# Kernel tuning notes

Hardware: AMD Instinct MI355X
Metric: run time of the kernel (lower is better)

The kernel has to match this reference:

```python
import jax, jax.numpy as jnp
import numpy as np

B, S, D, H, V, C = 64, 512, 512, 512, 32000, 1000
FF = 1024

def setup_inputs() -> dict:
    key = jax.random.key(0)
    ks = jax.random.split(key, 12)
    s = 0.02
    return {
        "tokens": jax.random.randint(ks[0], (B, S), 0, V),
        "emb": jax.random.normal(ks[1], (V, D), jnp.float32) * s,
        "Wx": jax.random.normal(ks[2], (D, H), jnp.float32) * s,
        "Wh": jax.random.normal(ks[3], (H, H), jnp.float32) * s,
        "b_rnn": jnp.zeros((H,), jnp.float32),
        "W1": jax.random.normal(ks[4], (H, FF), jnp.float32) * s,
        "b1": jnp.zeros((FF,), jnp.float32),
        "W2": jax.random.normal(ks[5], (FF, FF), jnp.float32) * s,
        "b2": jnp.zeros((FF,), jnp.float32),
        "Wo": jax.random.normal(ks[6], (FF, C), jnp.float32) * s,
        "bo": jnp.zeros((C,), jnp.float32),
    }

def reference(tokens, emb, Wx, Wh, b_rnn, W1, b1, W2, b2, Wo, bo):
    # Embedding with mask_zero=True: token 0 is a masked timestep
    x = emb[tokens]                                   # [B,S,D]
    mask = (tokens != 0)                              # [B,S]
    # Precompute input projection for all timesteps (hoisted out of the scan)
    xproj = jnp.einsum('bsd,dh->bsh', x, Wx) + b_rnn  # [B,S,H]

    def step(h, inp):
        xp, m = inp                                   # [B,H], [B]
        h_new = jax.nn.relu(xp + h @ Wh)
        # Keras masking: masked steps carry previous state forward
        h = jnp.where(m[:, None], h_new, h)
        return h, None

    h0 = jnp.zeros((B, H), xproj.dtype)
    h, _ = jax.lax.scan(step, h0, (xproj.transpose(1, 0, 2), mask.T))

    y = jax.nn.relu(h @ W1 + b1)
    y = jax.nn.relu(y @ W2 + b2)
    return jax.nn.softmax(y @ Wo + bo, axis=-1)       # [B,C]
```

## Files before the change

### kernel.cpp

```cpp
#include <hip/hip_runtime.h>
#include <stdint.h>

typedef _Float16 half2_t __attribute__((ext_vector_type(2)));
typedef short bf16x8 __attribute__((ext_vector_type(8)));
typedef float f32x4 __attribute__((ext_vector_type(4)));
typedef int i32x4 __attribute__((ext_vector_type(4)));
typedef int i32x8 __attribute__((ext_vector_type(8)));
typedef unsigned short u16;
typedef unsigned int u32;
typedef unsigned long long u64;

#define B_ 64
#define S_ 512
#define D_ 512
#define H_ 512
#define FF_ 1024
#define C_ 1000
#define V_ 32000

#define SW4 128.0f
#define SH4 256.0f

__device__ __forceinline__ u16 f2bf(float f){
  u32 u = __builtin_bit_cast(u32, f);
  u = (u + 0x7FFFu + ((u >> 16) & 1u)) >> 16;
  return (u16)u;
}
__device__ __forceinline__ u32 pkbf(float a, float b){
  return (u32)f2bf(a) | ((u32)f2bf(b) << 16);
}
__device__ __forceinline__ u32 packh2(float a, float b){
  u16 lo = __builtin_bit_cast(u16, (_Float16)a);
  u16 hi = __builtin_bit_cast(u16, (_Float16)b);
  return (u32)lo | ((u32)hi << 16);
}
__device__ __forceinline__ float fdot2u(u32 a, u32 b, float c){
  return __builtin_amdgcn_fdot2(__builtin_bit_cast(half2_t, a),
                                __builtin_bit_cast(half2_t, b), c, false);
}
__device__ __forceinline__ float h2f(u16 h){
  return (float)__builtin_bit_cast(_Float16, h);
}
__device__ __forceinline__ float fp4val(u32 c){
  int e = (c >> 1) & 3;
  float m = 1.0f + 0.5f * (float)(c & 1);
  return (e == 0) ? 0.5f * (float)(c & 1) : m * (float)(1 << (e - 1));
}

__global__ void k_prep(const float* __restrict__ Wx, u16* __restrict__ WxT,
                       const float* __restrict__ Wh, uint4* __restrict__ Wf4,
                       const float* __restrict__ W1, u32* __restrict__ W1p,
                       const float* __restrict__ W2, u32* __restrict__ W2p,
                       const float* __restrict__ Wo, u32* __restrict__ Wop){
  __shared__ u16 t[64][65];
  int bid = blockIdx.x, tid = threadIdx.x;
  if (bid < 64){
    int bx = bid & 7, by = bid >> 3;
    int c = tid & 63, r0 = (tid >> 6) * 16;
    #pragma unroll
    for (int i = 0; i < 16; i++){
      int k = by * 64 + r0 + i, n = bx * 64 + c;
      t[r0 + i][c] = f2bf(Wx[k * 512 + n]);
    }
    __syncthreads();
    #pragma unroll
    for (int i = 0; i < 16; i++){
      int n = bx * 64 + r0 + i, k = by * 64 + c;
      WxT[n * 512 + k] = t[c][r0 + i];
    }
  } else if (bid < 96){
    int g = (bid - 64) * 256 + tid;
    int fidx = g >> 6, l = g & 63;
    int wv = fidx >> 4, ct = (fidx >> 2) & 3, kt = fidx & 3;
    int q = l >> 4, n = wv * 64 + ct * 16 + (l & 15);
    int k0 = kt * 128 + q * 32;
    u32 d[4] = {0u, 0u, 0u, 0u};
    #pragma unroll
    for (int j = 0; j < 32; j++){
      float w = Wh[(size_t)(k0 + j) * 512 + n] * SW4;
      float aw = fabsf(w);
      u32 s = (w < 0.f) ? 8u : 0u;
      u32 c;
      if (aw < 2.f) c = (u32)(int)rintf(aw * 2.f);
      else if (aw < 4.f) c = 4u + (u32)(int)rintf(aw - 2.f);
      else { c = 6u + (u32)(int)rintf((aw - 4.f) * 0.5f); if (c > 7u) c = 7u; }
      d[j >> 3] |= (c | s) << (4 * (j & 7));
    }
    uint4 o; o.x = d[0]; o.y = d[1]; o.z = d[2]; o.w = d[3];
    Wf4[(size_t)fidx * 64 + l] = o;
  } else if (bid < 1120){
    int b2 = bid - 96;
    int p = b2 >> 2, n = (b2 & 3) * 256 + tid;
    W1p[p * FF_ + n] = packh2(W1[(2 * p) * FF_ + n], W1[(2 * p + 1) * FF_ + n]);
  } else if (bid < 3168){
    int b2 = bid - 1120;
    int p = b2 >> 2, n = (b2 & 3) * 256 + tid;
    W2p[p * FF_ + n] = packh2(W2[(2 * p) * FF_ + n], W2[(2 * p + 1) * FF_ + n]);
  } else {
    int b2 = bid - 3168;
    int p = b2 >> 2, n = (b2 & 3) * 256 + tid;
    if (n < C_)
      Wop[p * C_ + n] = packh2(Wo[(2 * p) * C_ + n], Wo[(2 * p + 1) * C_ + n]);
  }
}

__global__ __launch_bounds__(512) void k_gemm(const float* __restrict__ emb,
                                              const u16* __restrict__ WxT,
                                              const float* __restrict__ bias,
                                              u16* __restrict__ xpV){
  __shared__ __align__(16) u16 As[64 * 40];
  int tid = threadIdx.x;
  int m0 = blockIdx.x * 64;
  int w = tid >> 6, l = tid & 63, kg = l >> 4, r16 = l & 15;
  const u16* bptr[4];
  #pragma unroll
  for (int ni = 0; ni < 4; ni++)
    bptr[ni] = WxT + (size_t)(w * 64 + ni * 16 + r16) * 512 + kg * 8;
  f32x4 acc[4][4];
  #pragma unroll
  for (int mi = 0; mi < 4; mi++)
    #pragma unroll
    for (int ni = 0; ni < 4; ni++) acc[mi][ni] = (f32x4){0.f, 0.f, 0.f, 0.f};
  int srow = tid >> 3, sk = (tid & 7) * 4;
  for (int kt = 0; kt < 16; kt++){
    float4 f = *(const float4*)(emb + (size_t)(m0 + srow) * 512 + kt * 32 + sk);
    u32 lo = pkbf(f.x, f.y), hi = pkbf(f.z, f.w);
    __syncthreads();
    uint2 st; st.x = lo; st.y = hi;
    *(uint2*)(As + srow * 40 + sk) = st;
    __syncthreads();
    bf16x8 bfr[4], af[4];
    #pragma unroll
    for (int ni = 0; ni < 4; ni++)
      bfr[ni] = *(const bf16x8*)(bptr[ni] + kt * 32);
    #pragma unroll
    for (int mi = 0; mi < 4; mi++)
      af[mi] = *(const bf16x8*)(As + (mi * 16 + r16) * 40 + kg * 8);
    #pragma unroll
    for (int mi = 0; mi < 4; mi++)
      #pragma unroll
      for (int ni = 0; ni < 4; ni++)
        acc[mi][ni] = __builtin_amdgcn_mfma_f32_16x16x32_bf16(af[mi], bfr[ni], acc[mi][ni], 0, 0, 0);
  }
  #pragma unroll
  for (int ni = 0; ni < 4; ni++){
    int col = w * 64 + ni * 16 + r16;
    float bb = bias[col];
    #pragma unroll
    for (int mi = 0; mi < 4; mi++){
      int mb = m0 + mi * 16 + kg * 4;
      #pragma unroll
      for (int r = 0; r < 4; r++){
        float v = (acc[mi][ni][r] + bb) * SH4;
        xpV[(size_t)(mb + r) * 512 + col] = __builtin_bit_cast(u16, (_Float16)v);
      }
    }
  }
}

__global__ __launch_bounds__(512, 2) void k_rnn(
    const uint4* __restrict__ Wf4, const u16* __restrict__ xpV,
    const int* __restrict__ tokens, u32* __restrict__ hpack){
  __shared__ __align__(16) unsigned char g4[2][256];
  __shared__ int toks[512];
  int b = blockIdx.x, tid = threadIdx.x;
  int wv = tid >> 6, l = tid & 63, q = l >> 4, n16 = l & 15;
  int col = wv * 64 + q * 16 + n16;

  i32x8 wgt[16];
  #pragma unroll
  for (int ct = 0; ct < 4; ct++)
    #pragma unroll
    for (int kt = 0; kt < 4; kt++){
      int fidx = (wv * 4 + ct) * 4 + kt;
      uint4 wl = Wf4[(size_t)fidx * 64 + l];
      i32x8 w8 = {(int)wl.x, (int)wl.y, (int)wl.z, (int)wl.w, 0, 0, 0, 0};
      wgt[ct * 4 + kt] = w8;
    }

  toks[tid] = tokens[b * 512 + tid];
  if (tid < 64) ((u32*)g4[0])[tid] = 0;
  __syncthreads();

  u16 xraw = xpV[(size_t)toks[0] * 512 + col];
  u32 greg = 0;

  #pragma unroll 1
  for (int t = 0; t < 512; t++){
    int tn = toks[t < 511 ? t + 1 : 0];
    u16 xnext = xpV[(size_t)tn * 512 + col];
    bool wr = toks[t] != 0;
    const unsigned char* gc = g4[t & 1];

    f32x4 acc0 = {0.f,0.f,0.f,0.f}, acc1 = {0.f,0.f,0.f,0.f};
    f32x4 acc2 = {0.f,0.f,0.f,0.f}, acc3 = {0.f,0.f,0.f,0.f};
    #pragma unroll
    for (int kt = 0; kt < 4; kt++){
      i32x4 av = *(const i32x4*)(gc + kt * 64 + q * 16);
      i32x8 a8 = {av[0], av[1], av[2], av[3], 0, 0, 0, 0};
      acc0 = __builtin_amdgcn_mfma_scale_f32_16x16x128_f8f6f4(
          a8, wgt[0 * 4 + kt], acc0, 4, 4, 0, 127, 0, 127);
      acc1 = __builtin_amdgcn_mfma_scale_f32_16x16x128_f8f6f4(
          a8, wgt[1 * 4 + kt], acc1, 4, 4, 0, 127, 0, 127);
      acc2 = __builtin_amdgcn_mfma_scale_f32_16x16x128_f8f6f4(
          a8, wgt[2 * 4 + kt], acc2, 4, 4, 0, 127, 0, 127);
      acc3 = __builtin_amdgcn_mfma_scale_f32_16x16x128_f8f6f4(
          a8, wgt[3 * 4 + kt], acc3, 4, 4, 0, 127, 0, 127);
    }

    float av = (q == 0) ? acc0[0] : (q == 1) ? acc1[0] : (q == 2) ? acc2[0] : acc3[0];
    float gn = fmaxf(fmaf(av, 1.0f / SW4, h2f(xraw)), 0.f);
    u32 code;
    if (gn < 2.f) code = (u32)(int)rintf(gn * 2.f);
    else if (gn < 4.f) code = 4u + (u32)(int)rintf(gn - 2.f);
    else { u32 c = 6u + (u32)(int)rintf((gn - 4.f) * 0.5f); code = c > 7u ? 7u : c; }
    u32 pc = (u32)__shfl_xor((int)code, 1);
    u32 byte = (n16 & 1) ? (pc | (code << 4)) : (code | (pc << 4));
    if (wr) greg = byte;
    if ((l & 1) == 0) g4[(t + 1) & 1][col >> 1] = (unsigned char)greg;
    xraw = xnext;
    __syncthreads();
  }

  if (tid < 256){
    u32 byte = g4[0][tid];
    float f0 = fp4val(byte & 15u) * (1.0f / SH4);
    float f1 = fp4val(byte >> 4) * (1.0f / SH4);
    hpack[b * 256 + tid] = packh2(f0, f1);
  }
}

__global__ __launch_bounds__(512) void k_tail(const u32* __restrict__ hpack,
    const u32* __restrict__ W1p, const float* __restrict__ b1v,
    const u32* __restrict__ W2p, const float* __restrict__ b2v,
    const u32* __restrict__ Wop, const float* __restrict__ bov,
    float* __restrict__ out){
  __shared__ __align__(16) u32 A0[256], A1[256];
  __shared__ __align__(16) u32 B0[512], B1[512];
  __shared__ __align__(16) u32 C0[512], C1[512];
  __shared__ float redm0[8], redm1[8], reds0[8], reds1[8];
  int ba = blockIdx.x * 2, bb = ba + 1;
  int tid = threadIdx.x, wv = tid >> 6;
  if (tid < 256){ A0[tid] = hpack[ba * 256 + tid]; A1[tid] = hpack[bb * 256 + tid]; }
  __syncthreads();

  float a00 = 0.f, a01 = 0.f, a10 = 0.f, a11 = 0.f;
  #pragma unroll 4
  for (int p = 0; p < 256; p += 2){
    u32 h00 = A0[p], h01 = A0[p + 1], h10 = A1[p], h11 = A1[p + 1];
    const u32* wp = W1p + (size_t)p * FF_ + tid;
    u32 w0 = wp[0], w1 = wp[512], w0b = wp[FF_], w1b = wp[FF_ + 512];
    a00 = fdot2u(w0, h00, a00);  a01 = fdot2u(w1, h00, a01);
    a10 = fdot2u(w0, h10, a10);  a11 = fdot2u(w1, h10, a11);
    a00 = fdot2u(w0b, h01, a00); a01 = fdot2u(w1b, h01, a01);
    a10 = fdot2u(w0b, h11, a10); a11 = fdot2u(w1b, h11, a11);
  }
  {
    float blo = b1v[tid], bhi = b1v[tid + 512];
    float y00 = fmaxf(a00 + blo, 0.f), y01 = fmaxf(a01 + bhi, 0.f);
    float y10 = fmaxf(a10 + blo, 0.f), y11 = fmaxf(a11 + bhi, 0.f);
    float o00 = __shfl_xor(y00, 1), o01 = __shfl_xor(y01, 1);
    float o10 = __shfl_xor(y10, 1), o11 = __shfl_xor(y11, 1);
    if (!(tid & 1)){
      int i = tid >> 1;
      B0[i] = packh2(y00, o00); B0[256 + i] = packh2(y01, o01);
      B1[i] = packh2(y10, o10); B1[256 + i] = packh2(y11, o11);
    }
  }
  __syncthreads();

  a00 = a01 = a10 = a11 = 0.f;
  #pragma unroll 4
  for (int p = 0; p < 512; p += 2){
    u32 h00 = B0[p], h01 = B0[p + 1], h10 = B1[p], h11 = B1[p + 1];
    const u32* wp = W2p + (size_t)p * FF_ + tid;
    u32 w0 = wp[0], w1 = wp[512], w0b = wp[FF_], w1b = wp[FF_ + 512];
    a00 = fdot2u(w0, h00, a00);  a01 = fdot2u(w1, h00, a01);
    a10 = fdot2u(w0, h10, a10);  a11 = fdot2u(w1, h10, a11);
    a00 = fdot2u(w0b, h01, a00); a01 = fdot2u(w1b, h01, a01);
    a10 = fdot2u(w0b, h11, a10); a11 = fdot2u(w1b, h11, a11);
  }
  {
    float blo = b2v[tid], bhi = b2v[tid + 512];
    float y00 = fmaxf(a00 + blo, 0.f), y01 = fmaxf(a01 + bhi, 0.f);
    float y10 = fmaxf(a10 + blo, 0.f), y11 = fmaxf(a11 + bhi, 0.f);
    float o00 = __shfl_xor(y00, 1), o01 = __shfl_xor(y01, 1);
    float o10 = __shfl_xor(y10, 1), o11 = __shfl_xor(y11, 1);
    if (!(tid & 1)){
      int i = tid >> 1;
      C0[i] = packh2(y00, o00); C0[256 + i] = packh2(y01, o01);
      C1[i] = packh2(y10, o10); C1[256 + i] = packh2(y11, o11);
    }
  }
  __syncthreads();

  int n1 = tid + 512;
  bool v1 = n1 < C_;
  int n1c = v1 ? n1 : 0;
  float z00 = 0.f, z01 = 0.f, z10 = 0.f, z11 = 0.f;
  #pragma unroll 4
  for (int p = 0; p < 512; p++){
    u32 y0 = C0[p], y1 = C1[p];
    u32 w0 = Wop[(size_t)p * C_ + tid], w1 = Wop[(size_t)p * C_ + n1c];
    z00 = fdot2u(w0, y0, z00); z01 = fdot2u(w1, y0, z01);
    z10 = fdot2u(w0, y1, z10); z11 = fdot2u(w1, y1, z11);
  }
  z00 += bov[tid]; z10 += bov[tid];
  z01 += bov[n1c]; z11 += bov[n1c];
  float mx0 = fmaxf(z00, v1 ? z01 : -1e30f);
  float mx1 = fmaxf(z10, v1 ? z11 : -1e30f);
  #pragma unroll
  for (int o = 1; o < 64; o <<= 1){
    mx0 = fmaxf(mx0, __shfl_xor(mx0, o));
    mx1 = fmaxf(mx1, __shfl_xor(mx1, o));
  }
  if ((tid & 63) == 0){ redm0[wv] = mx0; redm1[wv] = mx1; }
  __syncthreads();
  mx0 = redm0[0]; mx1 = redm1[0];
  #pragma unroll
  for (int i = 1; i < 8; i++){
    mx0 = fmaxf(mx0, redm0[i]);
    mx1 = fmaxf(mx1, redm1[i]);
  }
  float e00 = __expf(z00 - mx0), e01 = v1 ? __expf(z01 - mx0) : 0.f;
  float e10 = __expf(z10 - mx1), e11 = v1 ? __expf(z11 - mx1) : 0.f;
  float s0 = e00 + e01, s1 = e10 + e11;
  #pragma unroll
  for (int o = 1; o < 64; o <<= 1){
    s0 += __shfl_xor(s0, o);
    s1 += __shfl_xor(s1, o);
  }
  if ((tid & 63) == 0){ reds0[wv] = s0; reds1[wv] = s1; }
  __syncthreads();
  s0 = 0.f; s1 = 0.f;
  #pragma unroll
  for (int i = 0; i < 8; i++){ s0 += reds0[i]; s1 += reds1[i]; }
  float inv0 = 1.0f / s0, inv1 = 1.0f / s1;
  out[(size_t)ba * C_ + tid] = e00 * inv0;
  out[(size_t)bb * C_ + tid] = e10 * inv1;
  if (v1){
    out[(size_t)ba * C_ + n1] = e01 * inv0;
    out[(size_t)bb * C_ + n1] = e11 * inv1;
  }
}

extern "C" void kernel_launch(void* const* d_in, const int* in_sizes, int n_in,
                              void* d_out, int out_size, void* d_ws, size_t ws_size,
                              hipStream_t stream) {
  const int*   tokens = (const int*)d_in[0];
  const float* emb    = (const float*)d_in[1];
  const float* Wx     = (const float*)d_in[2];
  const float* Wh     = (const float*)d_in[3];
  const float* brnn   = (const float*)d_in[4];
  const float* W1     = (const float*)d_in[5];
  const float* b1     = (const float*)d_in[6];
  const float* W2     = (const float*)d_in[7];
  const float* b2     = (const float*)d_in[8];
  const float* Wo     = (const float*)d_in[9];
  const float* bo     = (const float*)d_in[10];
  float* out = (float*)d_out;

  char* ws = (char*)d_ws;
  size_t off = 0;
  auto alloc = [&](size_t bytes) -> void* {
    void* p = ws + off;
    off += (bytes + 255) & ~(size_t)255;
    return p;
  };
  u16* WxT    = (u16*)alloc((size_t)512 * 512 * 2);
  u16* xpV    = (u16*)alloc((size_t)V_ * 512 * 2);
  uint4* Wf4  = (uint4*)alloc((size_t)128 * 64 * 16);
  u32* W1p    = (u32*)alloc((size_t)256 * 1024 * 4);
  u32* W2p    = (u32*)alloc((size_t)512 * 1024 * 4);
  u32* Wop    = (u32*)alloc((size_t)512 * 1000 * 4);
  u32* hpack  = (u32*)alloc((size_t)64 * 256 * 4);

  k_prep<<<dim3(5216), dim3(256), 0, stream>>>(Wx, WxT, Wh, Wf4,
                                               W1, W1p, W2, W2p, Wo, Wop);
  k_gemm<<<dim3(500), dim3(512), 0, stream>>>(emb, WxT, brnn, xpV);
  k_rnn<<<dim3(64), dim3(512), 0, stream>>>(Wf4, xpV, tokens, hpack);
  k_tail<<<dim3(32), dim3(512), 0, stream>>>(hpack, W1p, b1, W2p, b2, Wop, bo, out);
}
```

Baseline: 413.2 us.

## Split tail MLP into multi-block kernels and fold weight packing into GEMM launch

The single 32-block tail kernel, which ran FC1, FC2, the output projection and the softmax serially per batch pair, is replaced by four kernels. Each layer now spreads its output columns over a 4x32 grid, followed by a separate softmax kernel, so more CUs share the weight streaming. Packing of W1/W2/Wo moves from k_prep into extra blocks of the embedding GEMM launch, so it runs alongside the GEMM, and the GEMM software-prefetches the next emb tile. The cost is extra launches and intermediate round-trips through global memory.

```diff
diff --git a/kernel.cpp b/kernel.cpp
--- a/kernel.cpp
+++ b/kernel.cpp
@@ -48,10 +48,7 @@
 }
 
 __global__ void k_prep(const float* __restrict__ Wx, u16* __restrict__ WxT,
-                       const float* __restrict__ Wh, uint4* __restrict__ Wf4,
-                       const float* __restrict__ W1, u32* __restrict__ W1p,
-                       const float* __restrict__ W2, u32* __restrict__ W2p,
-                       const float* __restrict__ Wo, u32* __restrict__ Wop){
+                       const float* __restrict__ Wh, uint4* __restrict__ Wf4){
   __shared__ u16 t[64][65];
   int bid = blockIdx.x, tid = threadIdx.x;
   if (bid < 64){
@@ -68,7 +65,7 @@
       int n = bx * 64 + r0 + i, k = by * 64 + c;
       WxT[n * 512 + k] = t[c][r0 + i];
     }
-  } else if (bid < 96){
+  } else {
     int g = (bid - 64) * 256 + tid;
     int fidx = g >> 6, l = g & 63;
     int wv = fidx >> 4, ct = (fidx >> 2) & 3, kt = fidx & 3;
@@ -88,29 +85,36 @@
     }
     uint4 o; o.x = d[0]; o.y = d[1]; o.z = d[2]; o.w = d[3];
     Wf4[(size_t)fidx * 64 + l] = o;
-  } else if (bid < 1120){
-    int b2 = bid - 96;
-    int p = b2 >> 2, n = (b2 & 3) * 256 + tid;
-    W1p[p * FF_ + n] = packh2(W1[(2 * p) * FF_ + n], W1[(2 * p + 1) * FF_ + n]);
-  } else if (bid < 3168){
-    int b2 = bid - 1120;
-    int p = b2 >> 2, n = (b2 & 3) * 256 + tid;
-    W2p[p * FF_ + n] = packh2(W2[(2 * p) * FF_ + n], W2[(2 * p + 1) * FF_ + n]);
-  } else {
-    int b2 = bid - 3168;
-    int p = b2 >> 2, n = (b2 & 3) * 256 + tid;
-    if (n < C_)
-      Wop[p * C_ + n] = packh2(Wo[(2 * p) * C_ + n], Wo[(2 * p + 1) * C_ + n]);
   }
 }
 
 __global__ __launch_bounds__(512) void k_gemm(const float* __restrict__ emb,
                                               const u16* __restrict__ WxT,
                                               const float* __restrict__ bias,
-                                              u16* __restrict__ xpV){
+                                              u16* __restrict__ xpV,
+                                              const float* __restrict__ W1, u32* __restrict__ W1p,
+                                              const float* __restrict__ W2, u32* __restrict__ W2p,
+                                              const float* __restrict__ Wo, u32* __restrict__ Wop){
   __shared__ __align__(16) u16 As[64 * 40];
-  int tid = threadIdx.x;
-  int m0 = blockIdx.x * 64;
+  int bid = blockIdx.x, tid = threadIdx.x;
+  if (bid >= 500){
+    if (bid < 1012){
+      int i = (bid - 500) * 512 + tid;
+      int p = i >> 10, n = i & 1023;
+      W1p[p * FF_ + n] = packh2(W1[(2 * p) * FF_ + n], W1[(2 * p + 1) * FF_ + n]);
+    } else if (bid < 2036){
+      int i = (bid - 1012) * 512 + tid;
+      int p = i >> 10, n = i & 1023;
+      W2p[p * FF_ + n] = packh2(W2[(2 * p) * FF_ + n], W2[(2 * p + 1) * FF_ + n]);
+    } else {
+      int i = (bid - 2036) * 512 + tid;
+      int p = i >> 10, n = i & 1023;
+      if (n < C_)
+        Wop[p * C_ + n] = packh2(Wo[(2 * p) * C_ + n], Wo[(2 * p + 1) * C_ + n]);
+    }
+    return;
+  }
+  int m0 = bid * 64;
   int w = tid >> 6, l = tid & 63, kg = l >> 4, r16 = l & 15;
   const u16* bptr[4];
   #pragma unroll
@@ -122,9 +126,12 @@
     #pragma unroll
     for (int ni = 0; ni < 4; ni++) acc[mi][ni] = (f32x4){0.f, 0.f, 0.f, 0.f};
   int srow = tid >> 3, sk = (tid & 7) * 4;
+  const float* ebase = emb + (size_t)(m0 + srow) * 512 + sk;
+  float4 f = *(const float4*)ebase;
   for (int kt = 0; kt < 16; kt++){
-    float4 f = *(const float4*)(emb + (size_t)(m0 + srow) * 512 + kt * 32 + sk);
     u32 lo = pkbf(f.x, f.y), hi = pkbf(f.z, f.w);
+    float4 fn;
+    if (kt < 15) fn = *(const float4*)(ebase + (kt + 1) * 32);
     __syncthreads();
     uint2 st; st.x = lo; st.y = hi;
     *(uint2*)(As + srow * 40 + sk) = st;
@@ -141,6 +148,7 @@
       #pragma unroll
       for (int ni = 0; ni < 4; ni++)
         acc[mi][ni] = __builtin_amdgcn_mfma_f32_16x16x32_bf16(af[mi], bfr[ni], acc[mi][ni], 0, 0, 0);
+    f = fn;
   }
   #pragma unroll
   for (int ni = 0; ni < 4; ni++){
@@ -230,118 +238,108 @@
   }
 }
 
-__global__ __launch_bounds__(512) void k_tail(const u32* __restrict__ hpack,
-    const u32* __restrict__ W1p, const float* __restrict__ b1v,
-    const u32* __restrict__ W2p, const float* __restrict__ b2v,
-    const u32* __restrict__ Wop, const float* __restrict__ bov,
-    float* __restrict__ out){
-  __shared__ __align__(16) u32 A0[256], A1[256];
-  __shared__ __align__(16) u32 B0[512], B1[512];
-  __shared__ __align__(16) u32 C0[512], C1[512];
-  __shared__ float redm0[8], redm1[8], reds0[8], reds1[8];
-  int ba = blockIdx.x * 2, bb = ba + 1;
-  int tid = threadIdx.x, wv = tid >> 6;
-  if (tid < 256){ A0[tid] = hpack[ba * 256 + tid]; A1[tid] = hpack[bb * 256 + tid]; }
-  __syncthreads();
-
-  float a00 = 0.f, a01 = 0.f, a10 = 0.f, a11 = 0.f;
-  #pragma unroll 4
-  for (int p = 0; p < 256; p += 2){
-    u32 h00 = A0[p], h01 = A0[p + 1], h10 = A1[p], h11 = A1[p + 1];
-    const u32* wp = W1p + (size_t)p * FF_ + tid;
-    u32 w0 = wp[0], w1 = wp[512], w0b = wp[FF_], w1b = wp[FF_ + 512];
-    a00 = fdot2u(w0, h00, a00);  a01 = fdot2u(w1, h00, a01);
-    a10 = fdot2u(w0, h10, a10);  a11 = fdot2u(w1, h10, a11);
-    a00 = fdot2u(w0b, h01, a00); a01 = fdot2u(w1b, h01, a01);
-    a10 = fdot2u(w0b, h11, a10); a11 = fdot2u(w1b, h11, a11);
-  }
-  {
-    float blo = b1v[tid], bhi = b1v[tid + 512];
-    float y00 = fmaxf(a00 + blo, 0.f), y01 = fmaxf(a01 + bhi, 0.f);
-    float y10 = fmaxf(a10 + blo, 0.f), y11 = fmaxf(a11 + bhi, 0.f);
-    float o00 = __shfl_xor(y00, 1), o01 = __shfl_xor(y01, 1);
-    float o10 = __shfl_xor(y10, 1), o11 = __shfl_xor(y11, 1);
-    if (!(tid & 1)){
-      int i = tid >> 1;
-      B0[i] = packh2(y00, o00); B0[256 + i] = packh2(y01, o01);
-      B1[i] = packh2(y10, o10); B1[256 + i] = packh2(y11, o11);
-    }
-  }
-  __syncthreads();
-
-  a00 = a01 = a10 = a11 = 0.f;
-  #pragma unroll 4
-  for (int p = 0; p < 512; p += 2){
-    u32 h00 = B0[p], h01 = B0[p + 1], h10 = B1[p], h11 = B1[p + 1];
-    const u32* wp = W2p + (size_t)p * FF_ + tid;
-    u32 w0 = wp[0], w1 = wp[512], w0b = wp[FF_], w1b = wp[FF_ + 512];
-    a00 = fdot2u(w0, h00, a00);  a01 = fdot2u(w1, h00, a01);
-    a10 = fdot2u(w0, h10, a10);  a11 = fdot2u(w1, h10, a11);
-    a00 = fdot2u(w0b, h01, a00); a01 = fdot2u(w1b, h01, a01);
-    a10 = fdot2u(w0b, h11, a10); a11 = fdot2u(w1b, h11, a11);
-  }
-  {
-    float blo = b2v[tid], bhi = b2v[tid + 512];
-    float y00 = fmaxf(a00 + blo, 0.f), y01 = fmaxf(a01 + bhi, 0.f);
-    float y10 = fmaxf(a10 + blo, 0.f), y11 = fmaxf(a11 + bhi, 0.f);
-    float o00 = __shfl_xor(y00, 1), o01 = __shfl_xor(y01, 1);
-    float o10 = __shfl_xor(y10, 1), o11 = __shfl_xor(y11, 1);
-    if (!(tid & 1)){
-      int i = tid >> 1;
-      C0[i] = packh2(y00, o00); C0[256 + i] = packh2(y01, o01);
-      C1[i] = packh2(y10, o10); C1[256 + i] = packh2(y11, o11);
-    }
-  }
-  __syncthreads();
-
-  int n1 = tid + 512;
-  bool v1 = n1 < C_;
-  int n1c = v1 ? n1 : 0;
-  float z00 = 0.f, z01 = 0.f, z10 = 0.f, z11 = 0.f;
-  #pragma unroll 4
+__global__ __launch_bounds__(256) void k_fc1(const u32* __restrict__ hpack,
+    const u32* __restrict__ W1p, const float* __restrict__ b1, u32* __restrict__ y1p){
+  __shared__ u32 h0[256], h1[256];
+  int nx = blockIdx.x, bp = blockIdx.y, tid = threadIdx.x;
+  int ba = bp * 2, bb = ba + 1;
+  int n = nx * 256 + tid;
+  h0[tid] = hpack[ba * 256 + tid];
+  h1[tid] = hpack[bb * 256 + tid];
+  __syncthreads();
+  float a0 = 0.f, a1 = 0.f;
+  #pragma unroll 8
+  for (int p = 0; p < 256; p++){
+    u32 w = W1p[p * FF_ + n];
+    a0 = fdot2u(w, h0[p], a0);
+    a1 = fdot2u(w, h1[p], a1);
+  }
+  float bbv = b1[n];
+  float y0 = fmaxf(a0 + bbv, 0.f), y1 = fmaxf(a1 + bbv, 0.f);
+  float o0 = __shfl_xor(y0, 1), o1 = __shfl_xor(y1, 1);
+  if (!(tid & 1)){
+    y1p[ba * 512 + (n >> 1)] = packh2(y0, o0);
+    y1p[bb * 512 + (n >> 1)] = packh2(y1, o1);
+  }
+}
+
+__global__ __launch_bounds__(256) void k_fc2(const u32* __restrict__ y1p,
+    const u32* __restrict__ W2p, const float* __restrict__ b2, u32* __restrict__ y2p){
+  __shared__ u32 h0[512], h1[512];
+  int nx = blockIdx.x, bp = blockIdx.y, tid = threadIdx.x;
+  int ba = bp * 2, bb = ba + 1;
+  int n = nx * 256 + tid;
+  h0[tid] = y1p[ba * 512 + tid];       h1[tid] = y1p[bb * 512 + tid];
+  h0[tid + 256] = y1p[ba * 512 + 256 + tid];
+  h1[tid + 256] = y1p[bb * 512 + 256 + tid];
+  __syncthreads();
+  float a0 = 0.f, a1 = 0.f;
+  #pragma unroll 8
   for (int p = 0; p < 512; p++){
-    u32 y0 = C0[p], y1 = C1[p];
-    u32 w0 = Wop[(size_t)p * C_ + tid], w1 = Wop[(size_t)p * C_ + n1c];
-    z00 = fdot2u(w0, y0, z00); z01 = fdot2u(w1, y0, z01);
-    z10 = fdot2u(w0, y1, z10); z11 = fdot2u(w1, y1, z11);
-  }
-  z00 += bov[tid]; z10 += bov[tid];
-  z01 += bov[n1c]; z11 += bov[n1c];
-  float mx0 = fmaxf(z00, v1 ? z01 : -1e30f);
-  float mx1 = fmaxf(z10, v1 ? z11 : -1e30f);
-  #pragma unroll
-  for (int o = 1; o < 64; o <<= 1){
-    mx0 = fmaxf(mx0, __shfl_xor(mx0, o));
-    mx1 = fmaxf(mx1, __shfl_xor(mx1, o));
-  }
-  if ((tid & 63) == 0){ redm0[wv] = mx0; redm1[wv] = mx1; }
-  __syncthreads();
-  mx0 = redm0[0]; mx1 = redm1[0];
-  #pragma unroll
-  for (int i = 1; i < 8; i++){
-    mx0 = fmaxf(mx0, redm0[i]);
-    mx1 = fmaxf(mx1, redm1[i]);
-  }
-  float e00 = __expf(z00 - mx0), e01 = v1 ? __expf(z01 - mx0) : 0.f;
-  float e10 = __expf(z10 - mx1), e11 = v1 ? __expf(z11 - mx1) : 0.f;
-  float s0 = e00 + e01, s1 = e10 + e11;
-  #pragma unroll
-  for (int o = 1; o < 64; o <<= 1){
-    s0 += __shfl_xor(s0, o);
-    s1 += __shfl_xor(s1, o);
-  }
-  if ((tid & 63) == 0){ reds0[wv] = s0; reds1[wv] = s1; }
-  __syncthreads();
-  s0 = 0.f; s1 = 0.f;
-  #pragma unroll
-  for (int i = 0; i < 8; i++){ s0 += reds0[i]; s1 += reds1[i]; }
-  float inv0 = 1.0f / s0, inv1 = 1.0f / s1;
-  out[(size_t)ba * C_ + tid] = e00 * inv0;
-  out[(size_t)bb * C_ + tid] = e10 * inv1;
-  if (v1){
-    out[(size_t)ba * C_ + n1] = e01 * inv0;
-    out[(size_t)bb * C_ + n1] = e11 * inv1;
-  }
+    u32 w = W2p[p * FF_ + n];
+    a0 = fdot2u(w, h0[p], a0);
+    a1 = fdot2u(w, h1[p], a1);
+  }
+  float bbv = b2[n];
+  float y0 = fmaxf(a0 + bbv, 0.f), y1 = fmaxf(a1 + bbv, 0.f);
+  float o0 = __shfl_xor(y0, 1), o1 = __shfl_xor(y1, 1);
+  if (!(tid & 1)){
+    y2p[ba * 512 + (n >> 1)] = packh2(y0, o0);
+    y2p[bb * 512 + (n >> 1)] = packh2(y1, o1);
+  }
+}
+
+__global__ __launch_bounds__(256) void k_outz(const u32* __restrict__ y2p,
+    const u32* __restrict__ Wop, const float* __restrict__ bo, float* __restrict__ z){
+  __shared__ u32 h0[512], h1[512];
+  int nx = blockIdx.x, bp = blockIdx.y, tid = threadIdx.x;
+  int ba = bp * 2, bb = ba + 1;
+  h0[tid] = y2p[ba * 512 + tid];       h1[tid] = y2p[bb * 512 + tid];
+  h0[tid + 256] = y2p[ba * 512 + 256 + tid];
+  h1[tid + 256] = y2p[bb * 512 + 256 + tid];
+  __syncthreads();
+  int n = nx * 250 + tid;
+  if (tid >= 250) return;
+  float a0 = 0.f, a1 = 0.f;
+  #pragma unroll 8
+  for (int p = 0; p < 512; p++){
+    u32 w = Wop[p * C_ + n];
+    a0 = fdot2u(w, h0[p], a0);
+    a1 = fdot2u(w, h1[p], a1);
+  }
+  float bbv = bo[n];
+  z[ba * C_ + n] = a0 + bbv;
+  z[bb * C_ + n] = a1 + bbv;
+}
+
+__global__ __launch_bounds__(256) void k_norm(const float* __restrict__ z,
+                                              float* __restrict__ out){
+  __shared__ float redm[4], reds[4];
+  int b = blockIdx.x, tid = threadIdx.x;
+  float z0 = z[b * C_ + tid];
+  float z1 = z[b * C_ + 256 + tid];
+  float z2 = z[b * C_ + 512 + tid];
+  bool v3 = (768 + tid) < C_;
+  float z3 = v3 ? z[b * C_ + 768 + tid] : -1e30f;
+  float mx = fmaxf(fmaxf(z0, z1), fmaxf(z2, z3));
+  #pragma unroll
+  for (int o = 1; o < 64; o <<= 1) mx = fmaxf(mx, __shfl_xor(mx, o));
+  if ((tid & 63) == 0) redm[tid >> 6] = mx;
+  __syncthreads();
+  mx = fmaxf(fmaxf(redm[0], redm[1]), fmaxf(redm[2], redm[3]));
+  float e0 = __expf(z0 - mx), e1 = __expf(z1 - mx), e2 = __expf(z2 - mx);
+  float e3 = v3 ? __expf(z3 - mx) : 0.f;
+  float s = e0 + e1 + e2 + e3;
+  #pragma unroll
+  for (int o = 1; o < 64; o <<= 1) s += __shfl_xor(s, o);
+  if ((tid & 63) == 0) reds[tid >> 6] = s;
+  __syncthreads();
+  s = reds[0] + reds[1] + reds[2] + reds[3];
+  float inv = 1.0f / s;
+  out[b * C_ + tid] = e0 * inv;
+  out[b * C_ + 256 + tid] = e1 * inv;
+  out[b * C_ + 512 + tid] = e2 * inv;
+  if (v3) out[b * C_ + 768 + tid] = e3 * inv;
 }
 
 extern "C" void kernel_launch(void* const* d_in, const int* in_sizes, int n_in,
@@ -374,10 +372,16 @@
   u32* W2p    = (u32*)alloc((size_t)512 * 1024 * 4);
   u32* Wop    = (u32*)alloc((size_t)512 * 1000 * 4);
   u32* hpack  = (u32*)alloc((size_t)64 * 256 * 4);
-
-  k_prep<<<dim3(5216), dim3(256), 0, stream>>>(Wx, WxT, Wh, Wf4,
+  u32* y1p    = (u32*)alloc((size_t)64 * 512 * 4);
+  u32* y2p    = (u32*)alloc((size_t)64 * 512 * 4);
+  float* zbuf = (float*)alloc((size_t)64 * 1000 * 4);
+
+  k_prep<<<dim3(96), dim3(256), 0, stream>>>(Wx, WxT, Wh, Wf4);
+  k_gemm<<<dim3(3060), dim3(512), 0, stream>>>(emb, WxT, brnn, xpV,
                                                W1, W1p, W2, W2p, Wo, Wop);
-  k_gemm<<<dim3(500), dim3(512), 0, stream>>>(emb, WxT, brnn, xpV);
   k_rnn<<<dim3(64), dim3(512), 0, stream>>>(Wf4, xpV, tokens, hpack);
-  k_tail<<<dim3(32), dim3(512), 0, stream>>>(hpack, W1p, b1, W2p, b2, Wop, bo, out);
-}
+  k_fc1<<<dim3(4, 32), dim3(256), 0, stream>>>(hpack, W1p, b1, y1p);
+  k_fc2<<<dim3(4, 32), dim3(256), 0, stream>>>(y1p, W2p, b2, y2p);
+  k_outz<<<dim3(4, 32), dim3(256), 0, stream>>>(y2p, Wop, bo, zbuf);
+  k_norm<<<dim3(64), dim3(256), 0, stream>>>(zbuf, out);
+}
```

New measurement: 386.5 us. -6.5%, faster.
